# Kernel tuning notes

Measured on AMD Instinct MI355X. Metric: run time of the kernel, lower is better.

Reference implementation:

```python
import jax, jax.numpy as jnp
import numpy as np

D, H = 64, 16
B, S = 4, 4096
PI = 3.1415  # constant used verbatim in the original code


def setup_inputs() -> dict:
    key = jax.random.key(0)
    ks = jax.random.split(key, 11)
    inp = {
        'query': jax.random.normal(ks[0], (B, S, D), dtype=jnp.float32),
        'key': jax.random.normal(ks[1], (B, S, D), dtype=jnp.float32),
        'value': jax.random.normal(ks[2], (B, S, D), dtype=jnp.float32),
        'attn_mask': jnp.zeros((1,), dtype=bool),
        # Linear weights stored as (in, out); y = x @ W + b
        'wq_w': jax.random.normal(ks[3], (D, D * H), dtype=jnp.float32) * 0.05,
        'wq_b': jnp.zeros((D * H,), dtype=jnp.float32),
        'wk_w': jax.random.normal(ks[4], (D, D * H), dtype=jnp.float32) * 0.05,
        'wk_b': jnp.zeros((D * H,), dtype=jnp.float32),
        'wv_w': jax.random.normal(ks[5], (D, D * H), dtype=jnp.float32) * 0.05,
        'wv_b': jnp.zeros((D * H,), dtype=jnp.float32),
        'dense_w': jax.random.normal(ks[6], (D * H, D), dtype=jnp.float32) * 0.05,
        'dense_b': jnp.zeros((D,), dtype=jnp.float32),
    }
    return inp


def reference(query, key, value, attn_mask, wq_w, wq_b, wk_w, wk_b, wv_w, wv_b, dense_w, dense_b):
    b, s, _ = query.shape
    # projections -> (B, S, H, D); einsum axis n = heads
    q = (query @ wq_w + wq_b).reshape(b, s, H, D)
    k = (key @ wk_w + wk_b).reshape(b, s, H, D)
    v = (value @ wv_w + wv_b).reshape(b, s, H, D)

    q = jax.nn.elu(q) + 1.0
    k = jax.nn.elu(k) + 1.0

    pos = PI * jnp.arange(s, dtype=query.dtype) / s  # (S,)
    qc_w = jnp.cos(pos)
    qs_w = jnp.sin(pos)
    kc_w = jnp.sin(pos)  # NB: original uses sin for k_cos too (faithful)
    ks_w = jnp.sin(pos)

    q_cos = q * qc_w[None, :, None, None]
    q_sin = q * qs_w[None, :, None, None]
    k_cos = k * kc_w[None, :, None, None]
    k_sin = k * ks_w[None, :, None, None]

    def lin_attn(qf, kf):
        kv = jnp.einsum('bsnx,bsnz->bnxz', kf, v)      # (B,H,D,D)
        return jnp.einsum('bsnx,bnxz->bsnz', qf, kv)   # (B,S,H,D)

    qkv = lin_attn(q, k)
    qkv_cos = lin_attn(q_cos, k_cos)
    qkv_sin = lin_attn(q_sin, k_sin)

    denom = 1.0 / (
        jnp.einsum('bsnd,bnd->bsn', q, k.sum(axis=1))
        + jnp.einsum('bsnd,bnd->bsn', q_cos, k_cos.sum(axis=1))
        + jnp.einsum('bsnd,bnd->bsn', q_sin, k_sin.sum(axis=1))
        + 1e-05
    )

    O = (qkv + qkv_cos + qkv_sin) * denom[..., None]   # (B,S,H,D)
    concat = O.reshape(b, s, H * D)
    return concat @ dense_w + dense_b
```

## Files before the change

### kernel.cpp

```cpp
#include <hip/hip_runtime.h>
#include <math.h>

#define BB 4
#define SS 4096
#define DD 64
#define HH 16
#define PI_C 3.1415f


typedef __attribute__((ext_vector_type(8))) short short8;
typedef __attribute__((ext_vector_type(4))) float f32x4;

#define MFMA(a, b, c) __builtin_amdgcn_mfma_f32_16x16x32_bf16(a, b, c, 0, 0, 0)

__device__ __forceinline__ short f2bf(float f) {
    union { float f; unsigned u; } v; v.f = f;
    unsigned r = v.u + 0x7FFFu + ((v.u >> 16) & 1u);
    return (short)(r >> 16);
}
__device__ __forceinline__ float bf2f(short s) {
    union { unsigned u; float f; } v;
    v.u = ((unsigned)(unsigned short)s) << 16;
    return v.f;
}
__device__ __forceinline__ short8 cvt8(float4 a, float4 b) {
    short8 r;
    r[0] = f2bf(a.x); r[1] = f2bf(a.y); r[2] = f2bf(a.z); r[3] = f2bf(a.w);
    r[4] = f2bf(b.x); r[5] = f2bf(b.y); r[6] = f2bf(b.z); r[7] = f2bf(b.w);
    return r;
}
__device__ __forceinline__ float elu1(float x) { return x > 0.f ? x + 1.f : __expf(x); }
__device__ __forceinline__ void st4(short* p, short a, short b, short c, short d) {
    union { uint2 u; short s[4]; } x;
    x.s[0] = a; x.s[1] = b; x.s[2] = c; x.s[3] = d;
    *reinterpret_cast<uint2*>(p) = x.u;
}

__global__ __launch_bounds__(256) void k_prep(
    const float* __restrict__ wq, const float* __restrict__ wk,
    const float* __restrict__ wv, const float* __restrict__ wd,
    short* __restrict__ dst)
{
    const int h = blockIdx.x, y = blockIdx.y, t = threadIdx.x;
    const float* src = (y == 0) ? wq : (y == 1) ? wk : (y == 2) ? wv : wd;
    const int rs = (y < 3) ? 1024 : 64;
    const size_t srcbase = (y < 3) ? (size_t)(h * 64) : (size_t)(h * 4096);
    short* dm = dst + (size_t)y * 65536 + (size_t)h * 4096;
#pragma unroll
    for (int j = 0; j < 4; ++j) {
        int idx = j * 1024 + t * 4;
        int r = idx >> 6, c = idx & 63;
        float4 v = *reinterpret_cast<const float4*>(src + (size_t)r * rs + srcbase + c);
        dm[(c + 0) * 64 + r] = f2bf(v.x);
        dm[(c + 1) * 64 + r] = f2bf(v.y);
        dm[(c + 2) * 64 + r] = f2bf(v.z);
        dm[(c + 3) * 64 + r] = f2bf(v.w);
    }
}

__global__ __launch_bounds__(256, 2) void k_phase1(
    const float* __restrict__ key, const float* __restrict__ value,
    const float* __restrict__ wk_b, const float* __restrict__ wv_b,
    const short* __restrict__ wkTb, const short* __restrict__ wvTb,
    float* __restrict__ pkv, float* __restrict__ pkvs,
    float* __restrict__ pks)
{
    const int chunk = blockIdx.x, h = blockIdx.y, b = blockIdx.z;
    const int t = threadIdx.x, w = t >> 6, l = t & 63;
    const int lane15 = l & 15, q8 = (l >> 4) * 8, q4 = (l >> 4) * 4;

    __shared__ short kT[64 * 72], vT[64 * 72], vsT[64 * 72];
    __shared__ float ssin[512];
    __shared__ float sbk[64], sbv[64];
    __shared__ float sred[512];

    short8 bkf[2][4], bvf[2][4];
    {
        const short* wkh = wkTb + (size_t)h * 4096;
        const short* wvh = wvTb + (size_t)h * 4096;
#pragma unroll
        for (int kss = 0; kss < 2; ++kss)
#pragma unroll
            for (int nt = 0; nt < 4; ++nt) {
                bkf[kss][nt] = *reinterpret_cast<const short8*>(wkh + (nt * 16 + lane15) * 64 + kss * 32 + q8);
                bvf[kss][nt] = *reinterpret_cast<const short8*>(wvh + (nt * 16 + lane15) * 64 + kss * 32 + q8);
            }
    }
    ssin[t]       = __sinf(PI_C * (float)(chunk * 512 + t)       * (1.f / 4096.f));
    ssin[t + 256] = __sinf(PI_C * (float)(chunk * 512 + t + 256) * (1.f / 4096.f));
    if (t < 64) sbk[t] = wk_b[h * 64 + t];
    else if (t < 128) sbv[t - 64] = wv_b[h * 64 + (t - 64)];

    float4 kf0, kf1, kf2, kf3, vf0, vf1, vf2, vf3;
    {
        const size_t g = ((size_t)b * SS + chunk * 512 + w * 16 + lane15) * 64 + q8;
        kf0 = *reinterpret_cast<const float4*>(key + g);
        kf1 = *reinterpret_cast<const float4*>(key + g + 4);
        kf2 = *reinterpret_cast<const float4*>(key + g + 32);
        kf3 = *reinterpret_cast<const float4*>(key + g + 36);
        vf0 = *reinterpret_cast<const float4*>(value + g);
        vf1 = *reinterpret_cast<const float4*>(value + g + 4);
        vf2 = *reinterpret_cast<const float4*>(value + g + 32);
        vf3 = *reinterpret_cast<const float4*>(value + g + 36);
    }

    f32x4 ckv[4], ckvs[4];
#pragma unroll
    for (int i = 0; i < 4; ++i) {
        ckv[i]  = (f32x4){0.f, 0.f, 0.f, 0.f};
        ckvs[i] = (f32x4){0.f, 0.f, 0.f, 0.f};
    }
    float aks = 0.f, akss = 0.f;
    __syncthreads();

    for (int it = 0; it < 8; ++it) {
        const int sbase = it * 64;
        f32x4 ckp[4], cvp[4];
#pragma unroll
        for (int i = 0; i < 4; ++i) {
            ckp[i] = (f32x4){0.f, 0.f, 0.f, 0.f};
            cvp[i] = (f32x4){0.f, 0.f, 0.f, 0.f};
        }
        {
            short8 ak0 = cvt8(kf0, kf1), ak1 = cvt8(kf2, kf3);
            short8 av0 = cvt8(vf0, vf1), av1 = cvt8(vf2, vf3);
#pragma unroll
            for (int nt = 0; nt < 4; ++nt) {
                ckp[nt] = MFMA(ak0, bkf[0][nt], ckp[nt]);
                cvp[nt] = MFMA(av0, bvf[0][nt], cvp[nt]);
                ckp[nt] = MFMA(ak1, bkf[1][nt], ckp[nt]);
                cvp[nt] = MFMA(av1, bvf[1][nt], cvp[nt]);
            }
        }
        const int srel = w * 16 + q4;
#pragma unroll
        for (int nt = 0; nt < 4; ++nt) {
            const int x = nt * 16 + lane15;
            const float bk = sbk[x], bv = sbv[x];
            short ek[4], ev[4], es[4];
#pragma unroll
            for (int r = 0; r < 4; ++r) {
                float kk = elu1(ckp[nt][r] + bk);
                float vv = cvp[nt][r] + bv;
                ek[r] = f2bf(kk);
                ev[r] = f2bf(vv);
                es[r] = f2bf(vv * ssin[sbase + srel + r]);
            }
            st4(&kT [x * 72 + srel], ek[0], ek[1], ek[2], ek[3]);
            st4(&vT [x * 72 + srel], ev[0], ev[1], ev[2], ev[3]);
            st4(&vsT[x * 72 + srel], es[0], es[1], es[2], es[3]);
        }
        __syncthreads();
        if (it < 7) {
            const size_t g = ((size_t)b * SS + chunk * 512 + (it + 1) * 64 + w * 16 + lane15) * 64 + q8;
            kf0 = *reinterpret_cast<const float4*>(key + g);
            kf1 = *reinterpret_cast<const float4*>(key + g + 4);
            kf2 = *reinterpret_cast<const float4*>(key + g + 32);
            kf3 = *reinterpret_cast<const float4*>(key + g + 36);
            vf0 = *reinterpret_cast<const float4*>(value + g);
            vf1 = *reinterpret_cast<const float4*>(value + g + 4);
            vf2 = *reinterpret_cast<const float4*>(value + g + 32);
            vf3 = *reinterpret_cast<const float4*>(value + g + 36);
        }
#pragma unroll
        for (int kstep = 0; kstep < 2; ++kstep) {
            const int so = kstep * 32;
            short8 aV  = *reinterpret_cast<const short8*>(&vT [(w * 16 + lane15) * 72 + so + q8]);
            short8 aVS = *reinterpret_cast<const short8*>(&vsT[(w * 16 + lane15) * 72 + so + q8]);
#pragma unroll
            for (int nt = 0; nt < 4; ++nt) {
                short8 bK = *reinterpret_cast<const short8*>(&kT[(nt * 16 + lane15) * 72 + so + q8]);
                ckv[nt]  = MFMA(aV,  bK, ckv[nt]);
                ckvs[nt] = MFMA(aVS, bK, ckvs[nt]);
            }
        }
        {
            short8 k0 = *reinterpret_cast<const short8*>(&kT[l * 72 + w * 16]);
            short8 k1 = *reinterpret_cast<const short8*>(&kT[l * 72 + w * 16 + 8]);
#pragma unroll
            for (int e = 0; e < 8; ++e) {
                float fa = bf2f(k0[e]), fb = bf2f(k1[e]);
                aks  += fa + fb;
                akss += fa * ssin[sbase + w * 16 + e] + fb * ssin[sbase + w * 16 + 8 + e];
            }
        }
        __syncthreads();
    }

    const int bh = b * HH + h;
    const size_t pbase = ((size_t)(chunk * 64) + bh) * 4096;
#pragma unroll
    for (int nt = 0; nt < 4; ++nt) {
        const int x = nt * 16 + lane15;
#pragma unroll
        for (int r = 0; r < 4; ++r) {
            const int z = w * 16 + q4 + r;
            pkv [pbase + z * 64 + x] = ckv[nt][r];
            pkvs[pbase + z * 64 + x] = ckvs[nt][r];
        }
    }
    sred[t] = aks; sred[256 + t] = akss;
    __syncthreads();
    if (t < 64) {
        pks[((size_t)(chunk * 64) + bh) * 128 + t] =
            sred[t] + sred[64 + t] + sred[128 + t] + sred[192 + t];
    } else if (t < 128) {
        int tt = t - 64;
        pks[((size_t)(chunk * 64) + bh) * 128 + t] =
            sred[256 + tt] + sred[320 + tt] + sred[384 + tt] + sred[448 + tt];
    }
}

__global__ __launch_bounds__(256) void k_reduce(
    const float* __restrict__ pkv, const float* __restrict__ pkvs,
    const float* __restrict__ pks,
    short* __restrict__ kvb, short* __restrict__ kvsb,
    float* __restrict__ ksums)
{
    const int blk = blockIdx.x, t = threadIdx.x;
    if (blk < 512) {
        const float* src = (blk < 256) ? pkv : pkvs;
        short* dst = (blk < 256) ? kvb : kvsb;
        const int o4 = (blk & 255) * 256 + t;
        float4 s = make_float4(0.f, 0.f, 0.f, 0.f);
#pragma unroll
        for (int c = 0; c < 8; ++c) {
            float4 v = reinterpret_cast<const float4*>(src + (size_t)c * 262144)[o4];
            s.x += v.x; s.y += v.y; s.z += v.z; s.w += v.w;
        }
        st4(dst + (size_t)o4 * 4, f2bf(s.x), f2bf(s.y), f2bf(s.z), f2bf(s.w));
    } else {
        const int g = (blk - 512) * 256 + t;
        float4 s = make_float4(0.f, 0.f, 0.f, 0.f);
#pragma unroll
        for (int c = 0; c < 8; ++c) {
            float4 v = reinterpret_cast<const float4*>(pks + (size_t)c * 8192)[g];
            s.x += v.x; s.y += v.y; s.z += v.z; s.w += v.w;
        }
        reinterpret_cast<float4*>(ksums)[g] = s;
    }
}

__global__ __launch_bounds__(256, 4) void k_phase2(
    const float* __restrict__ query, const float* __restrict__ wq_b,
    const short* __restrict__ wqTb,
    const short* __restrict__ kvb, const short* __restrict__ kvsb,
    const float* __restrict__ ksums,
    const short* __restrict__ wdTb, const float* __restrict__ dense_b,
    float* __restrict__ out)
{
    const int st = blockIdx.x, b = blockIdx.y;
    const int s0 = st * 16;
    const int t = threadIdx.x, w = t >> 6, l = t & 63;
    const int lane15 = l & 15, q8 = (l >> 4) * 8, q4 = (l >> 4) * 4;
    const int x = w * 16 + lane15;

    __shared__ short sqin[16 * 72], sqp[16 * 72], sO[16 * 72];
    __shared__ float sbq[1024];
    __shared__ float sks2[128];
    __shared__ float scc[16], sdb[64];

    if (t < 128) {
        int row = t >> 3, c8 = (t & 7) * 8;
        const float* qp = query + ((size_t)b * SS + s0 + row) * 64 + c8;
        float4 f0 = *reinterpret_cast<const float4*>(qp);
        float4 f1 = *reinterpret_cast<const float4*>(qp + 4);
        *reinterpret_cast<short8*>(&sqin[row * 72 + c8]) = cvt8(f0, f1);
    }
    for (int i = t; i < 1024; i += 256) sbq[i] = wq_b[i];
    if (t < 16) {
        float p = PI_C * (float)(s0 + t) * (1.f / 4096.f);
        scc[t] = __cosf(p) + __sinf(p);
    }
    if (t >= 192) sdb[t - 192] = dense_b[t - 192];
    f32x4 cd = (f32x4){0.f, 0.f, 0.f, 0.f};
    __syncthreads();

    for (int h = 0; h < HH; ++h) {
        const size_t bh = (size_t)(b * HH + h);
        if (t < 128) sks2[t] = ksums[bh * 128 + t];

        f32x4 cq = (f32x4){0.f, 0.f, 0.f, 0.f};
        const short* wqh = wqTb + bh % HH * 0 + (size_t)h * 4096;
#pragma unroll
        for (int kss = 0; kss < 2; ++kss) {
            short8 a = *reinterpret_cast<const short8*>(&sqin[lane15 * 72 + kss * 32 + q8]);
            short8 bb = *reinterpret_cast<const short8*>(wqh + x * 64 + kss * 32 + q8);
            cq = MFMA(a, bb, cq);
        }
        short8 nb1[2], nb2[2];
#pragma unroll
        for (int kss = 0; kss < 2; ++kss) {
            nb1[kss] = *reinterpret_cast<const short8*>(kvb  + bh * 4096 + x * 64 + kss * 32 + q8);
            nb2[kss] = *reinterpret_cast<const short8*>(kvsb + bh * 4096 + x * 64 + kss * 32 + q8);
        }
        {
            const float bq = sbq[h * 64 + x];
#pragma unroll
            for (int r = 0; r < 4; ++r)
                sqp[(q4 + r) * 72 + x] = f2bf(elu1(cq[r] + bq));
        }
        __syncthreads();

        float invd;
        {
            const int sl = l >> 2;
            const int x0 = (l & 3) * 16;
            const float ccs = scc[sl];
            short8 qa = *reinterpret_cast<const short8*>(&sqp[sl * 72 + x0]);
            short8 qb = *reinterpret_cast<const short8*>(&sqp[sl * 72 + x0 + 8]);
            float dsum = 0.f;
#pragma unroll
            for (int e = 0; e < 8; ++e) {
                dsum += bf2f(qa[e]) * (sks2[x0 + e]     + ccs * sks2[64 + x0 + e]);
                dsum += bf2f(qb[e]) * (sks2[x0 + 8 + e] + ccs * sks2[64 + x0 + 8 + e]);
            }
            dsum += __shfl_xor(dsum, 1);
            dsum += __shfl_xor(dsum, 2);
            invd = 1.f / (dsum + 1e-5f);
        }
        float invq[4], ccq[4];
#pragma unroll
        for (int r = 0; r < 4; ++r) {
            invq[r] = __shfl(invd, (q4 + r) * 4);
            ccq[r]  = scc[q4 + r];
        }

        f32x4 ckv = (f32x4){0.f, 0.f, 0.f, 0.f};
        f32x4 ckvs = (f32x4){0.f, 0.f, 0.f, 0.f};
#pragma unroll
        for (int kss = 0; kss < 2; ++kss) {
            short8 a = *reinterpret_cast<const short8*>(&sqp[lane15 * 72 + kss * 32 + q8]);
            ckv  = MFMA(a, nb1[kss], ckv);
            ckvs = MFMA(a, nb2[kss], ckvs);
        }
        short8 dbf[2];
#pragma unroll
        for (int kss = 0; kss < 2; ++kss)
            dbf[kss] = *reinterpret_cast<const short8*>(wdTb + (size_t)h * 4096 + x * 64 + kss * 32 + q8);
#pragma unroll
        for (int r = 0; r < 4; ++r) {
            float o = (ckv[r] + ccq[r] * ckvs[r]) * invq[r];
            sO[(q4 + r) * 72 + x] = f2bf(o);
        }
        __syncthreads();

#pragma unroll
        for (int kss = 0; kss < 2; ++kss) {
            short8 a = *reinterpret_cast<const short8*>(&sO[lane15 * 72 + kss * 32 + q8]);
            cd = MFMA(a, dbf[kss], cd);
        }
    }

    {
        const float bias = sdb[x];
#pragma unroll
        for (int r = 0; r < 4; ++r)
            out[((size_t)b * SS + s0 + q4 + r) * 64 + x] = cd[r] + bias;
    }
}

extern "C" void kernel_launch(void* const* d_in, const int* in_sizes, int n_in,
                              void* d_out, int out_size, void* d_ws, size_t ws_size,
                              hipStream_t stream) {
    const float* query   = (const float*)d_in[0];
    const float* key     = (const float*)d_in[1];
    const float* value   = (const float*)d_in[2];
    const float* wq_w    = (const float*)d_in[4];
    const float* wq_b    = (const float*)d_in[5];
    const float* wk_w    = (const float*)d_in[6];
    const float* wk_b    = (const float*)d_in[7];
    const float* wv_w    = (const float*)d_in[8];
    const float* wv_b    = (const float*)d_in[9];
    const float* dense_w = (const float*)d_in[10];
    const float* dense_b = (const float*)d_in[11];
    float* out = (float*)d_out;

    char* ws = (char*)d_ws;
    float* pkv   = (float*)(ws);
    float* pkvs  = (float*)(ws + 8388608);
    float* pks   = (float*)(ws + 16777216);
    short* kvb   = (short*)(ws + 17039360);
    short* kvsb  = (short*)(ws + 17563648);
    float* ksums = (float*)(ws + 18087936);
    short* wT    = (short*)(ws + 18120704);
    short* wqTb  = wT;
    short* wkTb  = wT + 65536;
    short* wvTb  = wT + 131072;
    short* wdTb  = wT + 196608;

    hipLaunchKernelGGL(k_prep, dim3(16, 4), dim3(256), 0, stream,
                       wq_w, wk_w, wv_w, dense_w, wT);
    hipLaunchKernelGGL(k_phase1, dim3(8, HH, BB), dim3(256), 0, stream,
                       key, value, wk_b, wv_b, wkTb, wvTb, pkv, pkvs, pks);
    hipLaunchKernelGGL(k_reduce, dim3(520), dim3(256), 0, stream,
                       pkv, pkvs, pks, kvb, kvsb, ksums);
    hipLaunchKernelGGL(k_phase2, dim3(256, BB), dim3(256), 0, stream,
                       query, wq_b, wqTb, kvb, kvsb, ksums, wdTb, dense_b, out);
}
```

Baseline: 174.0 us.

## Split heads across waves in phase2 to remove per-head block barriers

Each wave now handles four heads on its own, computing all 64 output columns per head with per-wave LDS scratch, rather than all four waves sharing each head and synchronizing twice per head. This removes 32 block-wide barriers and the shared staging of biases and ksums, which are now read directly from global memory. Partial dense outputs are reduced across waves through LDS at the end. In exchange each wave does 4x more MFMAs per head and uses more registers and LDS, which could lower occupancy.

```diff
diff --git a/kernel.cpp b/kernel.cpp
--- a/kernel.cpp
+++ b/kernel.cpp
@@ -253,12 +253,10 @@
     const int s0 = st * 16;
     const int t = threadIdx.x, w = t >> 6, l = t & 63;
     const int lane15 = l & 15, q8 = (l >> 4) * 8, q4 = (l >> 4) * 4;
-    const int x = w * 16 + lane15;
-
-    __shared__ short sqin[16 * 72], sqp[16 * 72], sO[16 * 72];
-    __shared__ float sbq[1024];
-    __shared__ float sks2[128];
-    __shared__ float scc[16], sdb[64];
+
+    __shared__ __align__(16) short sqin[16 * 72];
+    __shared__ __align__(16) short swork[4][2][16 * 72];
+    __shared__ float scc[16];
 
     if (t < 128) {
         int row = t >> 3, c8 = (t & 7) * 8;
@@ -267,96 +265,136 @@
         float4 f1 = *reinterpret_cast<const float4*>(qp + 4);
         *reinterpret_cast<short8*>(&sqin[row * 72 + c8]) = cvt8(f0, f1);
     }
-    for (int i = t; i < 1024; i += 256) sbq[i] = wq_b[i];
     if (t < 16) {
         float p = PI_C * (float)(s0 + t) * (1.f / 4096.f);
         scc[t] = __cosf(p) + __sinf(p);
     }
-    if (t >= 192) sdb[t - 192] = dense_b[t - 192];
-    f32x4 cd = (f32x4){0.f, 0.f, 0.f, 0.f};
+    f32x4 cd[4];
+#pragma unroll
+    for (int i = 0; i < 4; ++i) cd[i] = (f32x4){0.f, 0.f, 0.f, 0.f};
     __syncthreads();
 
-    for (int h = 0; h < HH; ++h) {
+    short8 aq0 = *reinterpret_cast<const short8*>(&sqin[lane15 * 72 + q8]);
+    short8 aq1 = *reinterpret_cast<const short8*>(&sqin[lane15 * 72 + 32 + q8]);
+    const float ccs = scc[lane15];
+    const float ccr = scc[l >> 2];
+    short* sqp = &swork[w][0][0];
+    short* sOw = &swork[w][1][0];
+
+#pragma unroll 2
+    for (int i = 0; i < 4; ++i) {
+        const int h = (i << 2) | w;
         const size_t bh = (size_t)(b * HH + h);
-        if (t < 128) sks2[t] = ksums[bh * 128 + t];
-
-        f32x4 cq = (f32x4){0.f, 0.f, 0.f, 0.f};
-        const short* wqh = wqTb + bh % HH * 0 + (size_t)h * 4096;
-#pragma unroll
-        for (int kss = 0; kss < 2; ++kss) {
-            short8 a = *reinterpret_cast<const short8*>(&sqin[lane15 * 72 + kss * 32 + q8]);
-            short8 bb = *reinterpret_cast<const short8*>(wqh + x * 64 + kss * 32 + q8);
-            cq = MFMA(a, bb, cq);
-        }
-        short8 nb1[2], nb2[2];
-#pragma unroll
-        for (int kss = 0; kss < 2; ++kss) {
-            nb1[kss] = *reinterpret_cast<const short8*>(kvb  + bh * 4096 + x * 64 + kss * 32 + q8);
-            nb2[kss] = *reinterpret_cast<const short8*>(kvsb + bh * 4096 + x * 64 + kss * 32 + q8);
-        }
+        const short* wqh = wqTb + (size_t)h * 4096;
+        const short* wdh = wdTb + (size_t)h * 4096;
+        const short* kv1 = kvb  + bh * 4096;
+        const short* kv2 = kvsb + bh * 4096;
+
+        f32x4 cq[4];
+#pragma unroll
+        for (int nt = 0; nt < 4; ++nt) cq[nt] = (f32x4){0.f, 0.f, 0.f, 0.f};
+#pragma unroll
+        for (int nt = 0; nt < 4; ++nt) {
+            short8 b0 = *reinterpret_cast<const short8*>(wqh + (nt * 16 + lane15) * 64 + q8);
+            short8 b1 = *reinterpret_cast<const short8*>(wqh + (nt * 16 + lane15) * 64 + 32 + q8);
+            cq[nt] = MFMA(b0, aq0, cq[nt]);
+            cq[nt] = MFMA(b1, aq1, cq[nt]);
+        }
+#pragma unroll
+        for (int nt = 0; nt < 4; ++nt) {
+            float4 bq = *reinterpret_cast<const float4*>(wq_b + h * 64 + nt * 16 + q4);
+            short e0 = f2bf(elu1(cq[nt][0] + bq.x));
+            short e1 = f2bf(elu1(cq[nt][1] + bq.y));
+            short e2 = f2bf(elu1(cq[nt][2] + bq.z));
+            short e3 = f2bf(elu1(cq[nt][3] + bq.w));
+            st4(&sqp[lane15 * 72 + nt * 16 + q4], e0, e1, e2, e3);
+        }
+
+        float invs;
         {
-            const float bq = sbq[h * 64 + x];
-#pragma unroll
-            for (int r = 0; r < 4; ++r)
-                sqp[(q4 + r) * 72 + x] = f2bf(elu1(cq[r] + bq));
-        }
-        __syncthreads();
-
-        float invd;
-        {
-            const int sl = l >> 2;
-            const int x0 = (l & 3) * 16;
-            const float ccs = scc[sl];
+            const int sl = l >> 2, x0 = (l & 3) * 16;
+            const float* kp = ksums + bh * 128 + x0;
+            float4 A0 = *reinterpret_cast<const float4*>(kp);
+            float4 A1 = *reinterpret_cast<const float4*>(kp + 4);
+            float4 A2 = *reinterpret_cast<const float4*>(kp + 8);
+            float4 A3 = *reinterpret_cast<const float4*>(kp + 12);
+            float4 B0 = *reinterpret_cast<const float4*>(kp + 64);
+            float4 B1 = *reinterpret_cast<const float4*>(kp + 68);
+            float4 B2 = *reinterpret_cast<const float4*>(kp + 72);
+            float4 B3 = *reinterpret_cast<const float4*>(kp + 76);
             short8 qa = *reinterpret_cast<const short8*>(&sqp[sl * 72 + x0]);
             short8 qb = *reinterpret_cast<const short8*>(&sqp[sl * 72 + x0 + 8]);
-            float dsum = 0.f;
-#pragma unroll
-            for (int e = 0; e < 8; ++e) {
-                dsum += bf2f(qa[e]) * (sks2[x0 + e]     + ccs * sks2[64 + x0 + e]);
-                dsum += bf2f(qb[e]) * (sks2[x0 + 8 + e] + ccs * sks2[64 + x0 + 8 + e]);
-            }
+#define DT(qv, ka, kb) (bf2f(qv) * ((ka) + ccr * (kb)))
+            float dsum =
+                DT(qa[0], A0.x, B0.x) + DT(qa[1], A0.y, B0.y) + DT(qa[2], A0.z, B0.z) + DT(qa[3], A0.w, B0.w) +
+                DT(qa[4], A1.x, B1.x) + DT(qa[5], A1.y, B1.y) + DT(qa[6], A1.z, B1.z) + DT(qa[7], A1.w, B1.w) +
+                DT(qb[0], A2.x, B2.x) + DT(qb[1], A2.y, B2.y) + DT(qb[2], A2.z, B2.z) + DT(qb[3], A2.w, B2.w) +
+                DT(qb[4], A3.x, B3.x) + DT(qb[5], A3.y, B3.y) + DT(qb[6], A3.z, B3.z) + DT(qb[7], A3.w, B3.w);
+#undef DT
             dsum += __shfl_xor(dsum, 1);
             dsum += __shfl_xor(dsum, 2);
-            invd = 1.f / (dsum + 1e-5f);
-        }
-        float invq[4], ccq[4];
-#pragma unroll
-        for (int r = 0; r < 4; ++r) {
-            invq[r] = __shfl(invd, (q4 + r) * 4);
-            ccq[r]  = scc[q4 + r];
-        }
-
-        f32x4 ckv = (f32x4){0.f, 0.f, 0.f, 0.f};
-        f32x4 ckvs = (f32x4){0.f, 0.f, 0.f, 0.f};
-#pragma unroll
-        for (int kss = 0; kss < 2; ++kss) {
-            short8 a = *reinterpret_cast<const short8*>(&sqp[lane15 * 72 + kss * 32 + q8]);
-            ckv  = MFMA(a, nb1[kss], ckv);
-            ckvs = MFMA(a, nb2[kss], ckvs);
-        }
-        short8 dbf[2];
-#pragma unroll
-        for (int kss = 0; kss < 2; ++kss)
-            dbf[kss] = *reinterpret_cast<const short8*>(wdTb + (size_t)h * 4096 + x * 64 + kss * 32 + q8);
-#pragma unroll
-        for (int r = 0; r < 4; ++r) {
-            float o = (ckv[r] + ccq[r] * ckvs[r]) * invq[r];
-            sO[(q4 + r) * 72 + x] = f2bf(o);
-        }
-        __syncthreads();
-
-#pragma unroll
-        for (int kss = 0; kss < 2; ++kss) {
-            short8 a = *reinterpret_cast<const short8*>(&sO[lane15 * 72 + kss * 32 + q8]);
-            cd = MFMA(a, dbf[kss], cd);
+            float invd = 1.f / (dsum + 1e-5f);
+            invs = __shfl(invd, lane15 << 2);
+        }
+
+        short8 qf0 = *reinterpret_cast<const short8*>(&sqp[lane15 * 72 + q8]);
+        short8 qf1 = *reinterpret_cast<const short8*>(&sqp[lane15 * 72 + 32 + q8]);
+        f32x4 cv1[4], cv2[4];
+#pragma unroll
+        for (int nt = 0; nt < 4; ++nt) {
+            cv1[nt] = (f32x4){0.f, 0.f, 0.f, 0.f};
+            cv2[nt] = (f32x4){0.f, 0.f, 0.f, 0.f};
+        }
+#pragma unroll
+        for (int nt = 0; nt < 4; ++nt) {
+            const short* a1 = kv1 + (nt * 16 + lane15) * 64;
+            const short* a2 = kv2 + (nt * 16 + lane15) * 64;
+            cv1[nt] = MFMA(*reinterpret_cast<const short8*>(a1 + q8),      qf0, cv1[nt]);
+            cv1[nt] = MFMA(*reinterpret_cast<const short8*>(a1 + 32 + q8), qf1, cv1[nt]);
+            cv2[nt] = MFMA(*reinterpret_cast<const short8*>(a2 + q8),      qf0, cv2[nt]);
+            cv2[nt] = MFMA(*reinterpret_cast<const short8*>(a2 + 32 + q8), qf1, cv2[nt]);
+        }
+#pragma unroll
+        for (int nt = 0; nt < 4; ++nt) {
+            short e0 = f2bf((cv1[nt][0] + ccs * cv2[nt][0]) * invs);
+            short e1 = f2bf((cv1[nt][1] + ccs * cv2[nt][1]) * invs);
+            short e2 = f2bf((cv1[nt][2] + ccs * cv2[nt][2]) * invs);
+            short e3 = f2bf((cv1[nt][3] + ccs * cv2[nt][3]) * invs);
+            st4(&sOw[lane15 * 72 + nt * 16 + q4], e0, e1, e2, e3);
+        }
+
+        short8 of0 = *reinterpret_cast<const short8*>(&sOw[lane15 * 72 + q8]);
+        short8 of1 = *reinterpret_cast<const short8*>(&sOw[lane15 * 72 + 32 + q8]);
+#pragma unroll
+        for (int nt = 0; nt < 4; ++nt) {
+            short8 d0 = *reinterpret_cast<const short8*>(wdh + (nt * 16 + lane15) * 64 + q8);
+            short8 d1 = *reinterpret_cast<const short8*>(wdh + (nt * 16 + lane15) * 64 + 32 + q8);
+            cd[nt] = MFMA(of0, d0, cd[nt]);
+            cd[nt] = MFMA(of1, d1, cd[nt]);
         }
     }
 
     {
-        const float bias = sdb[x];
-#pragma unroll
-        for (int r = 0; r < 4; ++r)
-            out[((size_t)b * SS + s0 + q4 + r) * 64 + x] = cd[r] + bias;
+        float* red = reinterpret_cast<float*>(&swork[w][0][0]);
+#pragma unroll
+        for (int nt = 0; nt < 4; ++nt)
+#pragma unroll
+            for (int r = 0; r < 4; ++r)
+                red[(q4 + r) * 68 + nt * 16 + lane15] = cd[nt][r];
+    }
+    __syncthreads();
+    {
+        const int row = t >> 4, c4 = (t & 15) * 4;
+        float4 s = make_float4(0.f, 0.f, 0.f, 0.f);
+#pragma unroll
+        for (int ww = 0; ww < 4; ++ww) {
+            const float* red = reinterpret_cast<const float*>(&swork[ww][0][0]);
+            float4 v = *reinterpret_cast<const float4*>(red + row * 68 + c4);
+            s.x += v.x; s.y += v.y; s.z += v.z; s.w += v.w;
+        }
+        float4 db = *reinterpret_cast<const float4*>(dense_b + c4);
+        s.x += db.x; s.y += db.y; s.z += db.z; s.w += db.w;
+        *reinterpret_cast<float4*>(out + ((size_t)b * SS + s0 + row) * 64 + c4) = s;
     }
 }
 
```

Measured after the change: 181.1 us. 1.04x slower.
